# Optimization experiments

Measured on AMD Instinct MI355X. Metric: run time of the kernel, lower is better.

The kernel has to match this reference:

```python
import jax, jax.numpy as jnp
import numpy as np

N_NODES = 100000
N_FEATURES = 256

def setup_inputs() -> dict:
    key = jax.random.key(0)
    k1, k2, k3 = jax.random.split(key, 3)
    input_term = jax.random.normal(k1, (N_NODES, N_FEATURES), dtype=jnp.float32)
    kipf_term = jax.random.normal(k2, (N_NODES, N_FEATURES), dtype=jnp.float32)
    lbda = jax.random.uniform(k3, (N_NODES,), dtype=jnp.float32)
    return {"input_term": input_term, "kipf_term": kipf_term, "lbda": lbda, "spar": 1}

def reference(input_term, kipf_term, lbda, spar):
    # Original (train_lbda == 1): -(input_term.T @ diag(lbda)).T + kipf_term
    # diag-matmul is mathematically a per-node (row) scale, so use a broadcast multiply.
    return kipf_term - lbda[:, None] * input_term
```

## Files before the change

kernel.cpp:

```cpp
#include <hip/hip_runtime.h>
#include <hip/hip_bf16.h>


__global__ __launch_bounds__(256) void damping_kernel(
    const float4* __restrict__ input4,
    const float4* __restrict__ kipf4,
    const float* __restrict__ lbda,
    float4* __restrict__ out4,
    int n4)
{
    int i = blockIdx.x * blockDim.x + threadIdx.x;
    if (i >= n4) return;
    int row = i >> 6;
    float l = lbda[row];
    float4 a = input4[i];
    float4 k = kipf4[i];
    float4 o;
    o.x = k.x - l * a.x;
    o.y = k.y - l * a.y;
    o.z = k.z - l * a.z;
    o.w = k.w - l * a.w;
    out4[i] = o;
}

extern "C" void kernel_launch(void* const* d_in, const int* in_sizes, int n_in,
                              void* d_out, int out_size, void* d_ws, size_t ws_size,
                              hipStream_t stream) {
    const float4* input4 = (const float4*)d_in[0];
    const float4* kipf4  = (const float4*)d_in[1];
    const float*  lbda   = (const float*)d_in[2];
    float4* out4 = (float4*)d_out;

    int n4 = out_size / 4;
    int block = 256;
    int grid = (n4 + block - 1) / block;
    damping_kernel<<<grid, block, 0, stream>>>(input4, kipf4, lbda, out4, n4);
}
```

Measured before the change: 245.9 us.

## Use grid-stride loop with 4x unrolled loads and nontemporal stores

Replaces the one-element-per-thread launch with a fixed 2048-block grid-stride loop. Each thread issues four independent 16-byte loads per input before computing, which raises memory-level parallelism. Outputs are written with nontemporal stores so they do not pollute the cache. This trades per-thread launch overhead and cache pollution for a fixed grid size that may underfill or overfill the device depending on CU count.

```diff
diff --git a/kernel.cpp b/kernel.cpp
--- a/kernel.cpp
+++ b/kernel.cpp
@@ -2,37 +2,61 @@
 #include <hip/hip_bf16.h>
 
 
-__global__ __launch_bounds__(256) void damping_kernel(
-    const float4* __restrict__ input4,
-    const float4* __restrict__ kipf4,
+typedef float v4f __attribute__((ext_vector_type(4)));
+
+#define BLOCK 256
+#define GRID  2048
+
+__global__ __launch_bounds__(BLOCK) void damping_kernel(
+    const v4f* __restrict__ input4,
+    const v4f* __restrict__ kipf4,
     const float* __restrict__ lbda,
-    float4* __restrict__ out4,
+    v4f* __restrict__ out4,
     int n4)
 {
+    const int stride = gridDim.x * blockDim.x;
     int i = blockIdx.x * blockDim.x + threadIdx.x;
-    if (i >= n4) return;
-    int row = i >> 6;
-    float l = lbda[row];
-    float4 a = input4[i];
-    float4 k = kipf4[i];
-    float4 o;
-    o.x = k.x - l * a.x;
-    o.y = k.y - l * a.y;
-    o.z = k.z - l * a.z;
-    o.w = k.w - l * a.w;
-    out4[i] = o;
+
+    for (; i + 3 * stride < n4; i += 4 * stride) {
+        const int i0 = i, i1 = i + stride, i2 = i + 2 * stride, i3 = i + 3 * stride;
+        v4f a0 = input4[i0];
+        v4f a1 = input4[i1];
+        v4f a2 = input4[i2];
+        v4f a3 = input4[i3];
+        v4f k0 = kipf4[i0];
+        v4f k1 = kipf4[i1];
+        v4f k2 = kipf4[i2];
+        v4f k3 = kipf4[i3];
+        float l0 = lbda[i0 >> 6];
+        float l1 = lbda[i1 >> 6];
+        float l2 = lbda[i2 >> 6];
+        float l3 = lbda[i3 >> 6];
+        v4f o0 = k0 - l0 * a0;
+        v4f o1 = k1 - l1 * a1;
+        v4f o2 = k2 - l2 * a2;
+        v4f o3 = k3 - l3 * a3;
+        __builtin_nontemporal_store(o0, &out4[i0]);
+        __builtin_nontemporal_store(o1, &out4[i1]);
+        __builtin_nontemporal_store(o2, &out4[i2]);
+        __builtin_nontemporal_store(o3, &out4[i3]);
+    }
+    for (; i < n4; i += stride) {
+        float l = lbda[i >> 6];
+        v4f a = input4[i];
+        v4f k = kipf4[i];
+        v4f o = k - l * a;
+        __builtin_nontemporal_store(o, &out4[i]);
+    }
 }
 
 extern "C" void kernel_launch(void* const* d_in, const int* in_sizes, int n_in,
                               void* d_out, int out_size, void* d_ws, size_t ws_size,
                               hipStream_t stream) {
-    const float4* input4 = (const float4*)d_in[0];
-    const float4* kipf4  = (const float4*)d_in[1];
-    const float*  lbda   = (const float*)d_in[2];
-    float4* out4 = (float4*)d_out;
+    const v4f* input4 = (const v4f*)d_in[0];
+    const v4f* kipf4  = (const v4f*)d_in[1];
+    const float* lbda = (const float*)d_in[2];
+    v4f* out4 = (v4f*)d_out;
 
     int n4 = out_size / 4;
-    int block = 256;
-    int grid = (n4 + block - 1) / block;
-    damping_kernel<<<grid, block, 0, stream>>>(input4, kipf4, lbda, out4, n4);
+    damping_kernel<<<GRID, BLOCK, 0, stream>>>(input4, kipf4, lbda, out4, n4);
 }
```

Result: slower. 270.9 us (+10.2%).
